# Performance work log

Hardware: AMD Instinct MI355X
Metric: run time of the kernel (lower is better)

The kernel has to match this reference:

```python
import jax, jax.numpy as jnp
import numpy as np

N_NODES = 131072
N_EDGES = 8388608
NUM_GRAPHS = 1024
GAMMA = 1.0


def setup_inputs() -> dict:
    key = jax.random.key(0)
    k1, k2, k3 = jax.random.split(key, 3)
    node_pos = jax.random.normal(k1, (N_NODES, 2), dtype=jnp.float32)
    full_edge_index = jax.random.randint(k2, (2, N_EDGES), 0, N_NODES, dtype=jnp.int64)
    batch_idx = jnp.sort(jax.random.randint(k3, (N_NODES,), 0, NUM_GRAPHS, dtype=jnp.int64))
    return {"node_pos": node_pos, "full_edge_index": full_edge_index, "batch_idx": batch_idx}


def reference(node_pos, full_edge_index, batch_idx):
    # gather edge endpoints: [E, 2] each
    start = node_pos[full_edge_index[0]]
    end = node_pos[full_edge_index[1]]
    # Euclidean length per edge, then exponential distance decay
    eu = jnp.linalg.norm(end - start, axis=1)          # [E]
    edge_occlusion = jnp.exp(-GAMMA * eu)              # [E]
    # scatter-sum per graph, keyed by graph id of the source node
    index = batch_idx[full_edge_index[0]]              # [E]
    graph_occlusion = jax.ops.segment_sum(edge_occlusion, index, num_segments=NUM_GRAPHS)
    # reduce = torch.mean over graphs
    return jnp.mean(graph_occlusion)
```

## Files before the change

### kernel.cpp

```cpp
#include <hip/hip_runtime.h>


#define N_EDGES_C 8388608
#define INV_NUM_GRAPHS (1.0f / 1024.0f)

__global__ __launch_bounds__(256) void occlusion_reduce(
    const float2* __restrict__ pos,
    const int*    __restrict__ src,
    const int*    __restrict__ dst,
    float*        __restrict__ out)
{
    const int tid    = blockIdx.x * blockDim.x + threadIdx.x;
    const int stride = gridDim.x * blockDim.x;

    const int4* __restrict__ src4 = reinterpret_cast<const int4*>(src);
    const int4* __restrict__ dst4 = reinterpret_cast<const int4*>(dst);
    const int n4 = N_EDGES_C / 4;

    float acc = 0.0f;
    for (int i = tid; i < n4; i += stride) {
        const int4 s = src4[i];
        const int4 d = dst4[i];

        float2 ps, pd;
        float dx, dy;

        ps = pos[s.x]; pd = pos[d.x];
        dx = pd.x - ps.x; dy = pd.y - ps.y;
        acc += __expf(-sqrtf(dx * dx + dy * dy));

        ps = pos[s.y]; pd = pos[d.y];
        dx = pd.x - ps.x; dy = pd.y - ps.y;
        acc += __expf(-sqrtf(dx * dx + dy * dy));

        ps = pos[s.z]; pd = pos[d.z];
        dx = pd.x - ps.x; dy = pd.y - ps.y;
        acc += __expf(-sqrtf(dx * dx + dy * dy));

        ps = pos[s.w]; pd = pos[d.w];
        dx = pd.x - ps.x; dy = pd.y - ps.y;
        acc += __expf(-sqrtf(dx * dx + dy * dy));
    }

    #pragma unroll
    for (int off = 32; off > 0; off >>= 1)
        acc += __shfl_down(acc, off, 64);

    __shared__ float wave_sums[4];
    const int lane = threadIdx.x & 63;
    const int wid  = threadIdx.x >> 6;
    if (lane == 0) wave_sums[wid] = acc;
    __syncthreads();

    if (threadIdx.x == 0) {
        float s = wave_sums[0] + wave_sums[1] + wave_sums[2] + wave_sums[3];
        atomicAdd(out, s * INV_NUM_GRAPHS);
    }
}

extern "C" void kernel_launch(void* const* d_in, const int* in_sizes, int n_in,
                              void* d_out, int out_size, void* d_ws, size_t ws_size,
                              hipStream_t stream) {
    const float* node_pos = (const float*)d_in[0];
    const int*   edge_idx = (const int*)d_in[1];

    const int E = in_sizes[1] / 2;
    const int* src = edge_idx;
    const int* dst = edge_idx + E;

    float* out = (float*)d_out;
    hipMemsetAsync(out, 0, sizeof(float), stream);

    const int block = 256;
    const int grid  = 2048;
    occlusion_reduce<<<grid, block, 0, stream>>>(
        reinterpret_cast<const float2*>(node_pos), src, dst, out);
}
```

Before: 156.0 us.

## Batch all index loads and gathers per thread, replace atomic with two-pass reduction

Each thread now loads all four of its int4 index groups up front with nontemporal loads, then issues all 32 position gathers before any math. This exposes more memory-level parallelism to hide gather latency. The single atomic accumulation and the memset are replaced by per-block partials in workspace plus a small final reduction kernel. The code hardcodes an exact thread-to-work mapping (4 groups per thread) and adds register pressure from 16 float2 pairs, which may lower occupancy.

Result: slower. 166.8 us (+7.0%).

```diff
diff --git a/kernel.cpp b/kernel.cpp
--- a/kernel.cpp
+++ b/kernel.cpp
@@ -1,61 +1,90 @@
 #include <hip/hip_runtime.h>
 
 
-#define N_EDGES_C 8388608
+#define N_EDGES_C   8388608
+#define GRID1       2048
+#define BLOCK1      256
+#define TOTAL_THR   (GRID1 * BLOCK1)
+#define N_GROUPS    (N_EDGES_C / 4)
+#define GROUPS_PER_THREAD (N_GROUPS / TOTAL_THR)
 #define INV_NUM_GRAPHS (1.0f / 1024.0f)
 
-__global__ __launch_bounds__(256) void occlusion_reduce(
+typedef int v4i __attribute__((ext_vector_type(4)));
+
+__global__ __launch_bounds__(BLOCK1) void occlusion_partial(
     const float2* __restrict__ pos,
-    const int*    __restrict__ src,
-    const int*    __restrict__ dst,
-    float*        __restrict__ out)
+    const v4i*    __restrict__ src4,
+    const v4i*    __restrict__ dst4,
+    float*        __restrict__ partials)
 {
-    const int tid    = blockIdx.x * blockDim.x + threadIdx.x;
-    const int stride = gridDim.x * blockDim.x;
+    const int tid = blockIdx.x * blockDim.x + threadIdx.x;
 
-    const int4* __restrict__ src4 = reinterpret_cast<const int4*>(src);
-    const int4* __restrict__ dst4 = reinterpret_cast<const int4*>(dst);
-    const int n4 = N_EDGES_C / 4;
+    v4i s[GROUPS_PER_THREAD], d[GROUPS_PER_THREAD];
+    #pragma unroll
+    for (int j = 0; j < GROUPS_PER_THREAD; ++j) {
+        s[j] = __builtin_nontemporal_load(&src4[tid + j * TOTAL_THR]);
+        d[j] = __builtin_nontemporal_load(&dst4[tid + j * TOTAL_THR]);
+    }
 
-    float acc = 0.0f;
-    for (int i = tid; i < n4; i += stride) {
-        const int4 s = src4[i];
-        const int4 d = dst4[i];
+    float2 ps[16], pd[16];
+    #pragma unroll
+    for (int j = 0; j < GROUPS_PER_THREAD; ++j) {
+        #pragma unroll
+        for (int k = 0; k < 4; ++k) {
+            ps[j * 4 + k] = pos[s[j][k]];
+            pd[j * 4 + k] = pos[d[j][k]];
+        }
+    }
 
-        float2 ps, pd;
+    float acc0 = 0.f, acc1 = 0.f, acc2 = 0.f, acc3 = 0.f;
+    #pragma unroll
+    for (int k = 0; k < 4; ++k) {
         float dx, dy;
-
-        ps = pos[s.x]; pd = pos[d.x];
-        dx = pd.x - ps.x; dy = pd.y - ps.y;
-        acc += __expf(-sqrtf(dx * dx + dy * dy));
-
-        ps = pos[s.y]; pd = pos[d.y];
-        dx = pd.x - ps.x; dy = pd.y - ps.y;
-        acc += __expf(-sqrtf(dx * dx + dy * dy));
-
-        ps = pos[s.z]; pd = pos[d.z];
-        dx = pd.x - ps.x; dy = pd.y - ps.y;
-        acc += __expf(-sqrtf(dx * dx + dy * dy));
-
-        ps = pos[s.w]; pd = pos[d.w];
-        dx = pd.x - ps.x; dy = pd.y - ps.y;
-        acc += __expf(-sqrtf(dx * dx + dy * dy));
+        dx = pd[k +  0].x - ps[k +  0].x;  dy = pd[k +  0].y - ps[k +  0].y;
+        acc0 += __expf(-sqrtf(dx * dx + dy * dy));
+        dx = pd[k +  4].x - ps[k +  4].x;  dy = pd[k +  4].y - ps[k +  4].y;
+        acc1 += __expf(-sqrtf(dx * dx + dy * dy));
+        dx = pd[k +  8].x - ps[k +  8].x;  dy = pd[k +  8].y - ps[k +  8].y;
+        acc2 += __expf(-sqrtf(dx * dx + dy * dy));
+        dx = pd[k + 12].x - ps[k + 12].x;  dy = pd[k + 12].y - ps[k + 12].y;
+        acc3 += __expf(-sqrtf(dx * dx + dy * dy));
     }
+    float acc = (acc0 + acc1) + (acc2 + acc3);
 
     #pragma unroll
     for (int off = 32; off > 0; off >>= 1)
         acc += __shfl_down(acc, off, 64);
 
-    __shared__ float wave_sums[4];
+    __shared__ float wave_sums[BLOCK1 / 64];
     const int lane = threadIdx.x & 63;
     const int wid  = threadIdx.x >> 6;
     if (lane == 0) wave_sums[wid] = acc;
     __syncthreads();
 
     if (threadIdx.x == 0) {
-        float s = wave_sums[0] + wave_sums[1] + wave_sums[2] + wave_sums[3];
-        atomicAdd(out, s * INV_NUM_GRAPHS);
+        partials[blockIdx.x] = (wave_sums[0] + wave_sums[1]) +
+                               (wave_sums[2] + wave_sums[3]);
     }
+}
+
+__global__ __launch_bounds__(256) void occlusion_final(
+    const float* __restrict__ partials,
+    float*       __restrict__ out)
+{
+    float a = 0.f;
+    #pragma unroll
+    for (int i = 0; i < GRID1 / 256; ++i)
+        a += partials[threadIdx.x + i * 256];
+
+    #pragma unroll
+    for (int off = 32; off > 0; off >>= 1)
+        a += __shfl_down(a, off, 64);
+
+    __shared__ float w[4];
+    if ((threadIdx.x & 63) == 0) w[threadIdx.x >> 6] = a;
+    __syncthreads();
+    if (threadIdx.x == 0)
+        out[0] = ((w[0] + w[1]) + (w[2] + w[3])) * INV_NUM_GRAPHS;
 }
 
 extern "C" void kernel_launch(void* const* d_in, const int* in_sizes, int n_in,
@@ -68,11 +97,13 @@
     const int* src = edge_idx;
     const int* dst = edge_idx + E;
 
+    float* partials = (float*)d_ws;
     float* out = (float*)d_out;
-    hipMemsetAsync(out, 0, sizeof(float), stream);
 
-    const int block = 256;
-    const int grid  = 2048;
-    occlusion_reduce<<<grid, block, 0, stream>>>(
-        reinterpret_cast<const float2*>(node_pos), src, dst, out);
+    occlusion_partial<<<GRID1, BLOCK1, 0, stream>>>(
+        reinterpret_cast<const float2*>(node_pos),
+        reinterpret_cast<const v4i*>(src),
+        reinterpret_cast<const v4i*>(dst),
+        partials);
+    occlusion_final<<<1, 256, 0, stream>>>(partials, out);
 }
```
